# Kernel tuning notes

Hardware: AMD Instinct MI355X
Metric: run time of the kernel (lower is better)

The kernel has to match this reference:

```python
import jax, jax.numpy as jnp
import numpy as np

N, E, NF, EF = 2048, 65536, 128, 64
HID, NH, HD, FF, L = 256, 8, 32, 1024, 4
OUT, MAXN = 1280, 4096


def setup_inputs() -> dict:
    key = jax.random.key(0)
    ks = iter(jax.random.split(key, 64))
    def rn(shape, s=0.02):
        return jax.random.normal(next(ks), shape, jnp.float32) * s
    inp = dict(
        node_features=jax.random.normal(next(ks), (N, NF), jnp.float32),
        edge_features=jax.random.normal(next(ks), (E, EF), jnp.float32),
        edge_index=jax.random.randint(next(ks), (2, E), 0, N),
        W_node=rn((NF, HID)), b_node=jnp.zeros((HID,)),
        W_edge=rn((EF, HID)), b_edge=jnp.zeros((HID,)),
        pos_emb=rn((MAXN, HID), 1.0),
        Wq=rn((L, HID, HID)), bq=jnp.zeros((L, HID)),
        Wk=rn((L, HID, HID)), bk=jnp.zeros((L, HID)),
        Wv=rn((L, HID, HID)), bv=jnp.zeros((L, HID)),
        Wo=rn((L, HID, HID)), bo=jnp.zeros((L, HID)),
        Wep=rn((L, HID, NH)), bep=jnp.zeros((L, NH)),
        Wf1=rn((L, HID, FF)), bf1=jnp.zeros((L, FF)),
        Wf2=rn((L, FF, HID)), bf2=jnp.zeros((L, HID)),
        g1=jnp.ones((L, HID)), be1=jnp.zeros((L, HID)),
        g2=jnp.ones((L, HID)), be2=jnp.zeros((L, HID)),
        g_ln=jnp.ones((HID,)), b_ln=jnp.zeros((HID,)),
        Wp1=rn((HID, HID)), bp1=jnp.zeros((HID,)),
        Wp2=rn((HID, 1)), bp2=jnp.zeros((1,)),
        Wo1=rn((3 * HID, 2 * HID)), bo1=jnp.zeros((2 * HID,)),
        Wo2=rn((2 * HID, OUT)), bo2=jnp.zeros((OUT,)),
    )
    return inp


def _ln(x, g, b, eps=1e-5):
    m = x.mean(-1, keepdims=True)
    v = ((x - m) ** 2).mean(-1, keepdims=True)
    return (x - m) * jax.lax.rsqrt(v + eps) * g + b


def reference(node_features, edge_features, edge_index, W_node, b_node, W_edge,
              b_edge, pos_emb, Wq, bq, Wk, bk, Wv, bv, Wo, bo, Wep, bep,
              Wf1, bf1, Wf2, bf2, g1, be1, g2, be2, g_ln, b_ln,
              Wp1, bp1, Wp2, bp2, Wo1, bo1, Wo2, bo2):
    n = node_features.shape[0]
    src, dst = edge_index[0], edge_index[1]
    scale = float(np.sqrt(HD))
    # node encoding + learned positional embedding (n <= max_nodes path)
    x = node_features @ W_node + b_node + pos_emb[:n]
    edge_attr = edge_features @ W_edge + b_edge  # [E, HID]
    # symmetric adjacency mask with self-loops
    adj = jnp.zeros((n, n), bool).at[src, dst].set(True).at[dst, src].set(True)
    adj = adj.at[jnp.arange(n), jnp.arange(n)].set(True)
    for i in range(L):
        Q = (x @ Wq[i] + bq[i]).reshape(n, NH, HD)
        K = (x @ Wk[i] + bk[i]).reshape(n, NH, HD)
        V = (x @ Wv[i] + bv[i]).reshape(n, NH, HD)
        scores = jnp.einsum('nhd,mhd->nmh', Q, K) / scale  # [n, n, NH]
        ebias = edge_attr @ Wep[i] + bep[i]  # [E, NH]
        scores = scores.at[src, dst].add(ebias)  # accumulating scatter, same as per-edge loop
        scores = jnp.where(adj[:, None, :], scores.transpose(0, 2, 1), -jnp.inf)  # [n, NH, n]
        attn = jax.nn.softmax(scores, axis=-1)
        ctx = jnp.einsum('nhm,mhd->nhd', attn, V).reshape(n, HID)
        a = ctx @ Wo[i] + bo[i]
        x = _ln(x + a, g1[i], be1[i])
        f = jax.nn.gelu(x @ Wf1[i] + bf1[i], approximate=False) @ Wf2[i] + bf2[i]
        x = _ln(x + f, g2[i], be2[i])
    x = _ln(x, g_ln, b_ln)
    # global pooling (batch=None path): mean / max / attention
    mean_p = x.mean(0, keepdims=True)
    max_p = x.max(0, keepdims=True)
    aw = jax.nn.softmax(jnp.tanh(x @ Wp1 + bp1) @ Wp2 + bp2, axis=0)  # [n, 1]
    attn_p = (x * aw).sum(0, keepdims=True)
    g = jnp.concatenate([mean_p, max_p, attn_p], axis=1)  # [1, 3*HID]
    out = jax.nn.relu(g @ Wo1 + bo1) @ Wo2 + bo2  # [1, OUT]
    return out
```

## Files before the change

### kernel.cpp

```cpp
#include <hip/hip_runtime.h>
#include <math.h>

#define NNODE 2048
#define NEDGE 65536
#define HIDN  256
#define NHEAD 8
#define HDIM  32
#define FFD   1024
#define NLAYER 4
#define OUTD  1280
#define NNZ_MAX (2*NEDGE + NNODE)

typedef __attribute__((ext_vector_type(8))) short bf16x8;
typedef __attribute__((ext_vector_type(4))) float f32x4;

__device__ __forceinline__ unsigned short f2b(float f) {
    unsigned u = __float_as_uint(f);
    unsigned r = (u + 0x7fffu + ((u >> 16) & 1u)) >> 16;
    return (unsigned short)r;
}
__device__ __forceinline__ float b2f(unsigned short u) {
    return __uint_as_float((unsigned)u << 16);
}

template<int K, int EPI, int OUT>
__global__ __launch_bounds__(256)
void mgemm(const unsigned short* __restrict__ A, const unsigned short* __restrict__ Bt,
           const float* __restrict__ bias, const float* __restrict__ extra,
           float* __restrict__ Cf, unsigned short* __restrict__ Cb,
           int M, int N, const float* __restrict__ Wp2, float* __restrict__ sred)
{
    __shared__ __align__(16) unsigned short As[2][32 * 40];
    __shared__ __align__(16) unsigned short Bs[2][64 * 40];
    int tid = threadIdx.x;
    int bm0 = blockIdx.y * 32, bn0 = blockIdx.x * 64;
    int wave = tid >> 6, lane = tid & 63;
    int wm = (wave >> 1) * 16;
    int wn = (wave & 1) * 32;
    int lrow = lane & 15, quad = lane >> 4;
    int brow = tid >> 2, koff = (tid & 3) * 8;
    int arow = (tid & 127) >> 2;
    bool doA = tid < 128;
    const unsigned short* ap = A  + (size_t)(bm0 + arow) * K + koff;
    const unsigned short* bp = Bt + (size_t)(bn0 + brow) * K + koff;
    uint4 av, bv;
    if (doA) av = *(const uint4*)ap;
    bv = *(const uint4*)bp;
    constexpr int NC = K / 32;
    if (doA) *(uint4*)(&As[0][arow*40 + koff]) = av;
    *(uint4*)(&Bs[0][brow*40 + koff]) = bv;
    __syncthreads();
    f32x4 acc[2] = {};
    #pragma unroll 8
    for (int c = 0; c < NC; ++c) {
        int cur = c & 1;
        if (c + 1 < NC) {
            if (doA) av = *(const uint4*)(ap + (c+1)*32);
            bv = *(const uint4*)(bp + (c+1)*32);
        }
        bf16x8 af = *(const bf16x8*)(&As[cur][(wm + lrow)*40 + quad*8]);
        bf16x8 b0 = *(const bf16x8*)(&Bs[cur][(wn + lrow)*40 + quad*8]);
        bf16x8 b1 = *(const bf16x8*)(&Bs[cur][(wn + 16 + lrow)*40 + quad*8]);
        acc[0] = __builtin_amdgcn_mfma_f32_16x16x32_bf16(af, b0, acc[0], 0, 0, 0);
        acc[1] = __builtin_amdgcn_mfma_f32_16x16x32_bf16(af, b1, acc[1], 0, 0, 0);
        if (c + 1 < NC) {
            if (doA) *(uint4*)(&As[cur^1][arow*40 + koff]) = av;
            *(uint4*)(&Bs[cur^1][brow*40 + koff]) = bv;
        }
        __syncthreads();
    }
    if (EPI == 4) {
        #pragma unroll
        for (int r = 0; r < 4; r++) {
            int row = bm0 + wm + quad*4 + r;
            float ps = 0.f;
            #pragma unroll
            for (int j = 0; j < 2; j++) {
                int col = bn0 + wn + j*16 + lrow;
                float v = tanhf(acc[j][r] + bias[col]);
                ps += v * Wp2[col];
            }
            ps += __shfl_xor(ps, 1);
            ps += __shfl_xor(ps, 2);
            ps += __shfl_xor(ps, 4);
            ps += __shfl_xor(ps, 8);
            if (lrow == 0) atomicAdd(&sred[row], ps);
        }
        return;
    }
    #pragma unroll
    for (int j = 0; j < 2; j++) {
        int col = bn0 + wn + j*16 + lrow;
        float bvv = bias[col];
        #pragma unroll
        for (int r = 0; r < 4; r++) {
            int row = bm0 + wm + quad*4 + r;
            float v = acc[j][r] + bvv;
            if (EPI == 1) v = 0.5f * v * (1.f + erff(v * 0.70710678118654752f));
            else if (EPI == 3) v += extra[(size_t)row*N + col];
            if (OUT == 0 || OUT == 2) Cf[(size_t)row*N + col] = v;
            if (OUT == 1 || OUT == 2) Cb[(size_t)row*N + col] = f2b(v);
        }
    }
}

__global__ __launch_bounds__(256)
void transpose_all(const float* __restrict__ Wq, const float* __restrict__ Wk,
                   const float* __restrict__ Wv, const float* __restrict__ Wo,
                   const float* __restrict__ Wf1, const float* __restrict__ Wf2,
                   const float* __restrict__ W_node, const float* __restrict__ Wp1,
                   unsigned short* __restrict__ WqkvT, unsigned short* __restrict__ WoT,
                   unsigned short* __restrict__ Wf1T, unsigned short* __restrict__ Wf2T,
                   unsigned short* __restrict__ WnT, unsigned short* __restrict__ Wp1T,
                   const float* __restrict__ nf, unsigned short* __restrict__ nf_b,
                   const float* __restrict__ bq, const float* __restrict__ bk,
                   const float* __restrict__ bv, float* __restrict__ bqkv)
{
    __shared__ unsigned short tile[32][33];
    int bid = blockIdx.x;
    if (bid >= 3168) {
        int t = (bid - 3168) * 256 + threadIdx.x;
        if (t < NNODE*128) {
            nf_b[t] = f2b(nf[t]);
        } else {
            int u = t - NNODE*128;
            if (u < NLAYER*768) {
                int l = u / 768, j = u % 768;
                float vv = (j < 256) ? bq[l*256 + j] : (j < 512 ? bk[l*256 + j - 256] : bv[l*256 + j - 512]);
                bqkv[u] = vv;
            }
        }
        return;
    }
    const float* s; unsigned short* d; int K, N, n0, k0;
    if (bid < 1024) {
        int mat = bid >> 6, rem = bid & 63;
        int m4 = mat & 3, l = mat >> 2;
        s = (m4 == 0 ? Wq : m4 == 1 ? Wk : m4 == 2 ? Wv : Wo) + (size_t)l * 65536;
        d = (m4 < 3) ? WqkvT + (size_t)l*196608 + (size_t)m4*65536
                     : WoT + (size_t)l*65536;
        K = 256; N = 256; n0 = (rem & 7) * 32; k0 = (rem >> 3) * 32;
    } else if (bid < 2048) {
        int idx = bid - 1024; int l = idx >> 8, rem = idx & 255;
        s = Wf1 + (size_t)l*262144; d = Wf1T + (size_t)l*262144;
        K = 256; N = 1024; n0 = (rem & 31) * 32; k0 = (rem >> 5) * 32;
    } else if (bid < 3072) {
        int idx = bid - 2048; int l = idx >> 8, rem = idx & 255;
        s = Wf2 + (size_t)l*262144; d = Wf2T + (size_t)l*262144;
        K = 1024; N = 256; n0 = (rem & 7) * 32; k0 = (rem >> 3) * 32;
    } else if (bid < 3104) {
        int rem = bid - 3072;
        s = W_node; d = WnT;
        K = 128; N = 256; n0 = (rem & 7) * 32; k0 = (rem >> 3) * 32;
    } else {
        int rem = bid - 3104;
        s = Wp1; d = Wp1T;
        K = 256; N = 256; n0 = (rem & 7) * 32; k0 = (rem >> 3) * 32;
    }
    int tx = threadIdx.x & 31, ty = threadIdx.x >> 5;
    #pragma unroll
    for (int i = 0; i < 4; i++)
        tile[ty + i*8][tx] = f2b(s[(size_t)(k0 + ty + i*8) * N + n0 + tx]);
    __syncthreads();
    #pragma unroll
    for (int i = 0; i < 4; i++)
        d[(size_t)(n0 + ty + i*8) * K + k0 + tx] = tile[tx][ty + i*8];
}

__global__ void adj_build(const int* __restrict__ src, const int* __restrict__ dst,
                          unsigned* __restrict__ adjbits)
{
    int t = blockIdx.x * blockDim.x + threadIdx.x;
    if (t < NEDGE) {
        int s = src[t], d = dst[t];
        atomicOr(&adjbits[(size_t)s*64 + (d >> 5)], 1u << (d & 31));
        atomicOr(&adjbits[(size_t)d*64 + (s >> 5)], 1u << (s & 31));
    }
    if (t < NNODE)
        atomicOr(&adjbits[(size_t)t*64 + (t >> 5)], 1u << (t & 31));
}

__global__ void row_rank(const unsigned* __restrict__ adjbits,
                         unsigned* __restrict__ rowcum, int* __restrict__ deg)
{
    int i = blockIdx.x * blockDim.x + threadIdx.x;
    if (i >= NNODE) return;
    unsigned c = 0;
    for (int w = 0; w < 64; w++) {
        rowcum[i*64 + w] = c;
        c += __popc(adjbits[i*64 + w]);
    }
    deg[i] = (int)c;
}

__global__ __launch_bounds__(256)
void scan_kernel(const int* __restrict__ deg, int* __restrict__ rowoff)
{
    __shared__ int part[256];
    int tid = threadIdx.x;
    int base = tid * 8;
    int local[8]; int s = 0;
    #pragma unroll
    for (int k = 0; k < 8; k++) { local[k] = s; s += deg[base + k]; }
    part[tid] = s;
    __syncthreads();
    for (int off = 1; off < 256; off <<= 1) {
        int v = (tid >= off) ? part[tid - off] : 0;
        __syncthreads();
        part[tid] += v;
        __syncthreads();
    }
    int pre = (tid == 0) ? 0 : part[tid - 1];
    #pragma unroll
    for (int k = 0; k < 8; k++) rowoff[base + k] = pre + local[k];
    if (tid == 255) rowoff[NNODE] = part[255];
}

__global__ __launch_bounds__(256)
void fill_cols(const unsigned* __restrict__ adjbits, const int* __restrict__ rowoff,
               const unsigned* __restrict__ rowcum, int* __restrict__ cols)
{
    int t = blockIdx.x * 256 + threadIdx.x;
    int i = t >> 6, w = t & 63;
    unsigned bits = adjbits[(size_t)i*64 + w];
    int base = rowoff[i] + (int)rowcum[(size_t)i*64 + w];
    while (bits) {
        int b = __ffs(bits) - 1;
        cols[base++] = w*32 + b;
        bits &= bits - 1;
    }
}

__global__ void wcomb_kernel(const float* __restrict__ W_edge, const float* __restrict__ b_edge,
                             const float* __restrict__ Wep, const float* __restrict__ bep,
                             float* __restrict__ Wcomb, float* __restrict__ bcomb)
{
    int t = blockIdx.x * blockDim.x + threadIdx.x;
    if (t < 64*32) {
        int k = t >> 5, lh = t & 31, l = lh >> 3, h = lh & 7;
        float acc = 0.f;
        for (int c = 0; c < HIDN; c++)
            acc += W_edge[k*HIDN + c] * Wep[l*HIDN*NHEAD + c*NHEAD + h];
        Wcomb[k*32 + lh] = acc;
    } else if (t < 64*32 + 32) {
        int lh = t - 64*32, l = lh >> 3, h = lh & 7;
        float acc = bep[l*NHEAD + h];
        for (int c = 0; c < HIDN; c++)
            acc += b_edge[c] * Wep[l*HIDN*NHEAD + c*NHEAD + h];
        bcomb[lh] = acc;
    }
}

__global__ __launch_bounds__(256)
void edge_bias_scatter(const float* __restrict__ ef, const float* __restrict__ Wcomb,
                       const float* __restrict__ bcomb,
                       const int* __restrict__ src, const int* __restrict__ dst,
                       const unsigned* __restrict__ adjbits,
                       const unsigned* __restrict__ rowcum,
                       const int* __restrict__ rowoff, float* __restrict__ bias_csr)
{
    __shared__ float Wl[64*32];
    __shared__ float bl[32];
    int tid = threadIdx.x;
    for (int k = tid; k < 64*32; k += 256) Wl[k] = Wcomb[k];
    if (tid < 32) bl[tid] = bcomb[tid];
    __syncthreads();
    int t = blockIdx.x * 256 + tid;
    int e = t >> 5, lh = t & 31;
    const float* f = ef + (size_t)e * 64;
    float acc = bl[lh];
    #pragma unroll
    for (int k = 0; k < 64; k++) acc += f[k] * Wl[k*32 + lh];
    int s = src[e], d = dst[e];
    unsigned wbits = adjbits[(size_t)s*64 + (d >> 5)];
    int rank = (int)rowcum[(size_t)s*64 + (d >> 5)] + __popc(wbits & ((1u << (d & 31)) - 1u));
    int slot = rowoff[s] + rank;
    atomicAdd(&bias_csr[(size_t)slot*32 + lh], acc);
}

__global__ __launch_bounds__(256)
void attn_kernel(const unsigned short* __restrict__ QKVb, const int* __restrict__ rowoff,
                 const int* __restrict__ cols, const float* __restrict__ bias_csr,
                 unsigned short* __restrict__ ctxb, int layer)
{
    __shared__ float mS[4][8], lS[4][8];
    __shared__ __align__(16) float accS[4][256];
    int i = blockIdx.x;
    int tid = threadIdx.x;
    int w = tid >> 6, lane = tid & 63;
    int h = lane >> 3;
    int off = lane * 4;
    ushort4 qu = *(const ushort4*)(QKVb + (size_t)i*768 + off);
    float4 qf = { b2f(qu.x), b2f(qu.y), b2f(qu.z), b2f(qu.w) };
    int start = rowoff[i], end = rowoff[i+1];
    int lh0 = layer * 8 + h;
    float m = -INFINITY, l = 0.f;
    float4 acc = {0.f, 0.f, 0.f, 0.f};
    for (int c0 = start + w; c0 < end; c0 += 256) {
        int myslot = c0 + 4*lane;
        int mycol = (myslot < end) ? cols[myslot] : 0;
        int lim = min(end, c0 + 256);
        int it = 0;
        for (int slot = c0; slot < lim; slot += 4, ++it) {
            int j = __shfl(mycol, it);
            ushort4 ku = *(const ushort4*)(QKVb + (size_t)j*768 + 256 + off);
            float s = qf.x*b2f(ku.x) + qf.y*b2f(ku.y) + qf.z*b2f(ku.z) + qf.w*b2f(ku.w);
            s += __shfl_xor(s, 1);
            s += __shfl_xor(s, 2);
            s += __shfl_xor(s, 4);
            s = s * 0.17677669529663687f + bias_csr[(size_t)slot*32 + lh0];
            float mn = fmaxf(m, s);
            float sc = __expf(m - mn);
            float p  = __expf(s - mn);
            ushort4 vu = *(const ushort4*)(QKVb + (size_t)j*768 + 512 + off);
            acc.x = acc.x*sc + p*b2f(vu.x);
            acc.y = acc.y*sc + p*b2f(vu.y);
            acc.z = acc.z*sc + p*b2f(vu.z);
            acc.w = acc.w*sc + p*b2f(vu.w);
            l = l*sc + p;
            m = mn;
        }
    }
    if ((lane & 7) == 0) { mS[w][h] = m; lS[w][h] = l; }
    *(float4*)&accS[w][off] = acc;
    __syncthreads();
    if (w == 0) {
        float m0 = mS[0][h], m1 = mS[1][h], m2 = mS[2][h], m3 = mS[3][h];
        float mx = fmaxf(fmaxf(m0, m1), fmaxf(m2, m3));
        float e0 = (m0 == -INFINITY) ? 0.f : __expf(m0 - mx);
        float e1 = (m1 == -INFINITY) ? 0.f : __expf(m1 - mx);
        float e2 = (m2 == -INFINITY) ? 0.f : __expf(m2 - mx);
        float e3 = (m3 == -INFINITY) ? 0.f : __expf(m3 - mx);
        float ls = lS[0][h]*e0 + lS[1][h]*e1 + lS[2][h]*e2 + lS[3][h]*e3;
        float4 a0 = *(float4*)&accS[0][off];
        float4 a1 = *(float4*)&accS[1][off];
        float4 a2 = *(float4*)&accS[2][off];
        float4 a3 = *(float4*)&accS[3][off];
        float inv = 1.f / ls;
        ushort4 o;
        o.x = f2b((a0.x*e0 + a1.x*e1 + a2.x*e2 + a3.x*e3) * inv);
        o.y = f2b((a0.y*e0 + a1.y*e1 + a2.y*e2 + a3.y*e3) * inv);
        o.z = f2b((a0.z*e0 + a1.z*e1 + a2.z*e2 + a3.z*e3) * inv);
        o.w = f2b((a0.w*e0 + a1.w*e1 + a2.w*e2 + a3.w*e3) * inv);
        *(ushort4*)(ctxb + (size_t)i*HIDN + off) = o;
    }
}

template<bool RES>
__global__ __launch_bounds__(256)
void ln_kernel(float* __restrict__ x, const float* __restrict__ r,
               const float* __restrict__ g, const float* __restrict__ b,
               unsigned short* __restrict__ xb)
{
    __shared__ float lds[4];
    int row = blockIdx.x, c = threadIdx.x;
    float v = x[(size_t)row*HIDN + c];
    if (RES) v += r[(size_t)row*HIDN + c];
    float s = v;
    for (int mm = 1; mm < 64; mm <<= 1) s += __shfl_xor(s, mm);
    if ((c & 63) == 0) lds[c >> 6] = s;
    __syncthreads();
    float mean = (lds[0] + lds[1] + lds[2] + lds[3]) * (1.f / HIDN);
    __syncthreads();
    float dv = v - mean;
    float qq = dv * dv;
    for (int mm = 1; mm < 64; mm <<= 1) qq += __shfl_xor(qq, mm);
    if ((c & 63) == 0) lds[c >> 6] = qq;
    __syncthreads();
    float var = (lds[0] + lds[1] + lds[2] + lds[3]) * (1.f / HIDN);
    float rs = rsqrtf(var + 1e-5f);
    float o = dv * rs * g[c] + b[c];
    x[(size_t)row*HIDN + c] = o;
    xb[(size_t)row*HIDN + c] = f2b(o);
}

__global__ __launch_bounds__(256)
void pool_part(const float* __restrict__ x, const float* __restrict__ sred,
               float* __restrict__ partial)
{
    __shared__ float red[4];
    __shared__ float aw[128];
    int b = blockIdx.x, tid = threadIdx.x;
    float mxs = -INFINITY;
    for (int r = tid; r < NNODE; r += 256) mxs = fmaxf(mxs, sred[r]);
    for (int mm = 1; mm < 64; mm <<= 1) mxs = fmaxf(mxs, __shfl_xor(mxs, mm));
    if ((tid & 63) == 0) red[tid >> 6] = mxs;
    __syncthreads();
    mxs = fmaxf(fmaxf(red[0], red[1]), fmaxf(red[2], red[3]));
    __syncthreads();
    float ss = 0.f;
    for (int r = tid; r < NNODE; r += 256) ss += __expf(sred[r] - mxs);
    for (int mm = 1; mm < 64; mm <<= 1) ss += __shfl_xor(ss, mm);
    if ((tid & 63) == 0) red[tid >> 6] = ss;
    __syncthreads();
    ss = red[0] + red[1] + red[2] + red[3];
    float inv = 1.f / ss;
    int r0 = b * 128;
    if (tid < 128) aw[tid] = __expf(sred[r0 + tid] - mxs) * inv;
    __syncthreads();
    float sm = 0.f, mx = -INFINITY, ap = 0.f;
    for (int r = 0; r < 128; r++) {
        float v = x[(size_t)(r0 + r)*HIDN + tid];
        sm += v;
        mx = fmaxf(mx, v);
        ap += v * aw[r];
    }
    partial[(size_t)b*768 + tid]       = sm;
    partial[(size_t)b*768 + 256 + tid] = mx;
    partial[(size_t)b*768 + 512 + tid] = ap;
}

__global__ __launch_bounds__(256)
void pool_fin(const float* __restrict__ partial, float* __restrict__ g)
{
    int c = threadIdx.x;
    float sm = 0.f, mx = -INFINITY, ap = 0.f;
    for (int b = 0; b < 16; b++) {
        sm += partial[(size_t)b*768 + c];
        mx = fmaxf(mx, partial[(size_t)b*768 + 256 + c]);
        ap += partial[(size_t)b*768 + 512 + c];
    }
    g[c]          = sm * (1.f / NNODE);
    g[HIDN + c]   = mx;
    g[2*HIDN + c] = ap;
}

__global__ __launch_bounds__(256)
void head1(const float* __restrict__ g, const float* __restrict__ Wo1,
           const float* __restrict__ bo1, float* __restrict__ h1)
{
    __shared__ float hp[4][64];
    int tid = threadIdx.x;
    int w = tid >> 6, lane = tid & 63;
    int j = blockIdx.x * 64 + lane;
    float acc = 0.f;
    int k0 = w * 192;
    for (int k = k0; k < k0 + 192; k++)
        acc += g[k] * Wo1[(size_t)k*512 + j];
    hp[w][lane] = acc;
    __syncthreads();
    if (w == 0) {
        float s = hp[0][lane] + hp[1][lane] + hp[2][lane] + hp[3][lane] + bo1[j];
        h1[j] = fmaxf(s, 0.f);
    }
}

__global__ __launch_bounds__(256)
void head2(const float* __restrict__ h1, const float* __restrict__ Wo2,
           const float* __restrict__ bo2, float* __restrict__ out)
{
    __shared__ float hp[4][64];
    int tid = threadIdx.x;
    int w = tid >> 6, lane = tid & 63;
    int j = blockIdx.x * 64 + lane;
    float acc = 0.f;
    int k0 = w * 128;
    for (int k = k0; k < k0 + 128; k++)
        acc += h1[k] * Wo2[(size_t)k*OUTD + j];
    hp[w][lane] = acc;
    __syncthreads();
    if (w == 0)
        out[j] = hp[0][lane] + hp[1][lane] + hp[2][lane] + hp[3][lane] + bo2[j];
}

extern "C" void kernel_launch(void* const* d_in, const int* in_sizes, int n_in,
                              void* d_out, int out_size, void* d_ws, size_t ws_size,
                              hipStream_t stream)
{
    const float* node_features = (const float*)d_in[0];
    const float* edge_features = (const float*)d_in[1];
    const int*   edge_index    = (const int*)d_in[2];
    const float* W_node = (const float*)d_in[3];
    const float* b_node = (const float*)d_in[4];
    const float* W_edge = (const float*)d_in[5];
    const float* b_edge = (const float*)d_in[6];
    const float* pos_emb = (const float*)d_in[7];
    const float* Wq = (const float*)d_in[8];
    const float* bq = (const float*)d_in[9];
    const float* Wk = (const float*)d_in[10];
    const float* bk = (const float*)d_in[11];
    const float* Wv = (const float*)d_in[12];
    const float* bv = (const float*)d_in[13];
    const float* Wo = (const float*)d_in[14];
    const float* bo = (const float*)d_in[15];
    const float* Wep = (const float*)d_in[16];
    const float* bep = (const float*)d_in[17];
    const float* Wf1 = (const float*)d_in[18];
    const float* bf1 = (const float*)d_in[19];
    const float* Wf2 = (const float*)d_in[20];
    const float* bf2 = (const float*)d_in[21];
    const float* g1  = (const float*)d_in[22];
    const float* be1 = (const float*)d_in[23];
    const float* g2  = (const float*)d_in[24];
    const float* be2 = (const float*)d_in[25];
    const float* g_ln = (const float*)d_in[26];
    const float* b_ln = (const float*)d_in[27];
    const float* Wp1 = (const float*)d_in[28];
    const float* bp1 = (const float*)d_in[29];
    const float* Wp2 = (const float*)d_in[30];
    const float* bp2 = (const float*)d_in[31];
    const float* Wo1 = (const float*)d_in[32];
    const float* bo1 = (const float*)d_in[33];
    const float* Wo2 = (const float*)d_in[34];
    const float* bo2 = (const float*)d_in[35];
    (void)bp2;
    const int* src = edge_index;
    const int* dst = edge_index + NEDGE;

    char* w = (char*)d_ws;
    auto carve = [&](size_t nbytes) {
        void* p = (void*)w;
        w += (nbytes + 255) & ~(size_t)255;
        return p;
    };
    float* x        = (float*)carve((size_t)NNODE*HIDN*4);
    unsigned short* xb = (unsigned short*)carve((size_t)NNODE*HIDN*2);
    unsigned short* bufQKVb = (unsigned short*)carve((size_t)NNODE*768*2);
    float* bufO     = (float*)carve((size_t)NNODE*HIDN*4);
    unsigned short* bufAb = (unsigned short*)carve((size_t)NNODE*HIDN*2);
    unsigned short* bufFb = (unsigned short*)carve((size_t)NNODE*FFD*2);
    float* Wcomb    = (float*)carve(64*32*4);
    float* bcomb    = (float*)carve(32*4);
    unsigned* adjbits = (unsigned*)carve((size_t)NNODE*64*4);
    float* bias_csr = (float*)carve((size_t)NNZ_MAX*32*4);
    float* sbuf  = (float*)carve(NNODE*4);
    unsigned* rowcum  = (unsigned*)carve((size_t)NNODE*64*4);
    int* deg    = (int*)carve(NNODE*4);
    int* rowoff = (int*)carve((NNODE+1)*4);
    int* colsb  = (int*)carve((size_t)NNZ_MAX*4);
    float* gbuf  = (float*)carve(3*HIDN*4);
    float* partial = (float*)carve(16*768*4);
    float* h1buf = (float*)carve(512*4);
    unsigned short* nf_b  = (unsigned short*)carve((size_t)NNODE*128*2);
    unsigned short* WnT   = (unsigned short*)carve((size_t)HIDN*128*2);
    unsigned short* WqkvT = (unsigned short*)carve((size_t)NLAYER*768*HIDN*2);
    float*          bqkv  = (float*)carve((size_t)NLAYER*768*4);
    unsigned short* WoT   = (unsigned short*)carve((size_t)NLAYER*HIDN*HIDN*2);
    unsigned short* Wf1T  = (unsigned short*)carve((size_t)NLAYER*FFD*HIDN*2);
    unsigned short* Wf2T  = (unsigned short*)carve((size_t)NLAYER*HIDN*FFD*2);
    unsigned short* Wp1T  = (unsigned short*)carve((size_t)HIDN*HIDN*2);

    hipMemsetAsync(adjbits, 0,
                   (size_t)NNODE*64*4 + (size_t)NNZ_MAX*32*4 + (size_t)NNODE*4, stream);
    adj_build<<<(NEDGE+255)/256, 256, 0, stream>>>(src, dst, adjbits);
    row_rank<<<NNODE/256, 256, 0, stream>>>(adjbits, rowcum, deg);
    scan_kernel<<<1, 256, 0, stream>>>(deg, rowoff);
    fill_cols<<<(NNODE*64)/256, 256, 0, stream>>>(adjbits, rowoff, rowcum, colsb);
    wcomb_kernel<<<(64*32+32+255)/256, 256, 0, stream>>>(W_edge, b_edge, Wep, bep, Wcomb, bcomb);
    edge_bias_scatter<<<(NEDGE*32)/256, 256, 0, stream>>>(
        edge_features, Wcomb, bcomb, src, dst, adjbits, rowcum, rowoff, bias_csr);

    transpose_all<<<3168 + 1024 + 12, 256, 0, stream>>>(
        Wq, Wk, Wv, Wo, Wf1, Wf2, W_node, Wp1,
        WqkvT, WoT, Wf1T, Wf2T, WnT, Wp1T,
        node_features, nf_b, bq, bk, bv, bqkv);

    mgemm<128,3,2><<<dim3(HIDN/64, NNODE/32), 256, 0, stream>>>(
        nf_b, WnT, b_node, pos_emb, x, xb, NNODE, HIDN, nullptr, nullptr);

    for (int l = 0; l < NLAYER; l++) {
        mgemm<256,0,1><<<dim3(768/64, NNODE/32), 256, 0, stream>>>(
            xb, WqkvT + (size_t)l*768*HIDN, bqkv + l*768, nullptr, nullptr, bufQKVb, NNODE, 768, nullptr, nullptr);
        attn_kernel<<<NNODE, 256, 0, stream>>>(bufQKVb, rowoff, colsb, bias_csr, bufAb, l);
        mgemm<256,0,0><<<dim3(HIDN/64, NNODE/32), 256, 0, stream>>>(
            bufAb, WoT + (size_t)l*HIDN*HIDN, bo + l*HIDN, nullptr, bufO, nullptr, NNODE, HIDN, nullptr, nullptr);
        ln_kernel<true><<<NNODE, 256, 0, stream>>>(x, bufO, g1 + l*HIDN, be1 + l*HIDN, xb);
        mgemm<256,1,1><<<dim3(FFD/64, NNODE/32), 256, 0, stream>>>(
            xb, Wf1T + (size_t)l*FFD*HIDN, bf1 + l*FFD, nullptr, nullptr, bufFb, NNODE, FFD, nullptr, nullptr);
        mgemm<1024,0,0><<<dim3(HIDN/64, NNODE/32), 256, 0, stream>>>(
            bufFb, Wf2T + (size_t)l*HIDN*FFD, bf2 + l*HIDN, nullptr, bufO, nullptr, NNODE, HIDN, nullptr, nullptr);
        ln_kernel<true><<<NNODE, 256, 0, stream>>>(x, bufO, g2 + l*HIDN, be2 + l*HIDN, xb);
    }

    ln_kernel<false><<<NNODE, 256, 0, stream>>>(x, nullptr, g_ln, b_ln, xb);
    mgemm<256,4,0><<<dim3(HIDN/64, NNODE/32), 256, 0, stream>>>(
        xb, Wp1T, bp1, nullptr, nullptr, nullptr, NNODE, HIDN, Wp2, sbuf);
    pool_part<<<16, 256, 0, stream>>>(x, sbuf, partial);
    pool_fin<<<1, 256, 0, stream>>>(partial, gbuf);
    head1<<<8, 256, 0, stream>>>(gbuf, Wo1, bo1, h1buf);
    head2<<<OUTD/64, 256, 0, stream>>>(h1buf, Wo2, bo2, (float*)d_out);
}
```

Before: 453.3 us.

## Fuse residual+LayerNorm into full-row GEMMs and prefetch K/V in attention

Adds a full-row-width (256-column) GEMM kernel that applies bias, the residual add and LayerNorm in its epilogue, including a double-LN variant for the final layer. This replaces the Wo and Wf2 GEMMs together with their separate LN kernels and the final LN launch, removing a round trip of the fp32 intermediate through memory and several launches. The attention loop is also software-pipelined so the next K/V rows and edge bias load while the current one is computed. The trade-off is fewer blocks (64 per GEMM) with lower parallelism and more register pressure.

Measured after the change: 496.7 us. 9.6% more time.

```diff
diff --git a/kernel.cpp b/kernel.cpp
--- a/kernel.cpp
+++ b/kernel.cpp
@@ -102,6 +102,187 @@
             if (OUT == 1 || OUT == 2) Cb[(size_t)row*N + col] = f2b(v);
         }
     }
+}
+
+template<int K, bool DBL>
+__global__ __launch_bounds__(256)
+void mgemm_wide(const unsigned short* __restrict__ A, const unsigned short* __restrict__ Bt,
+                const float* __restrict__ bias, const float* __restrict__ res,
+                const float* __restrict__ ga, const float* __restrict__ ba,
+                const float* __restrict__ gb, const float* __restrict__ bb,
+                float* __restrict__ X, unsigned short* __restrict__ Xb)
+{
+    __shared__ __align__(16) unsigned short As[2][32 * 40];
+    __shared__ __align__(16) unsigned short Bs[2][256 * 40];
+    __shared__ float rsum[4][32], rsq[4][32], rsum2[4][32], rsq2[4][32];
+    int tid = threadIdx.x;
+    int bm0 = blockIdx.x * 32;
+    int w = tid >> 6, lane = tid & 63;
+    int lrow = lane & 15, quad = lane >> 4;
+    int wn = w * 64;
+    int brow = tid >> 2, koff = (tid & 3) * 8;
+    int arow = (tid & 127) >> 2;
+    bool doA = tid < 128;
+    const unsigned short* ap = A + (size_t)(bm0 + arow) * K + koff;
+    const unsigned short* bp0 = Bt + (size_t)brow * K + koff;
+    const unsigned short* bp1 = Bt + (size_t)(brow + 64) * K + koff;
+    const unsigned short* bp2 = Bt + (size_t)(brow + 128) * K + koff;
+    const unsigned short* bp3 = Bt + (size_t)(brow + 192) * K + koff;
+    uint4 av, bv0, bv1, bv2, bv3;
+    if (doA) av = *(const uint4*)ap;
+    bv0 = *(const uint4*)bp0;
+    bv1 = *(const uint4*)bp1;
+    bv2 = *(const uint4*)bp2;
+    bv3 = *(const uint4*)bp3;
+    constexpr int NC = K / 32;
+    if (doA) *(uint4*)(&As[0][arow*40 + koff]) = av;
+    *(uint4*)(&Bs[0][brow*40 + koff])        = bv0;
+    *(uint4*)(&Bs[0][(brow+64)*40 + koff])   = bv1;
+    *(uint4*)(&Bs[0][(brow+128)*40 + koff])  = bv2;
+    *(uint4*)(&Bs[0][(brow+192)*40 + koff])  = bv3;
+    __syncthreads();
+    f32x4 acc[2][4] = {};
+    #pragma unroll 8
+    for (int c = 0; c < NC; ++c) {
+        int cur = c & 1;
+        if (c + 1 < NC) {
+            if (doA) av = *(const uint4*)(ap + (c+1)*32);
+            bv0 = *(const uint4*)(bp0 + (c+1)*32);
+            bv1 = *(const uint4*)(bp1 + (c+1)*32);
+            bv2 = *(const uint4*)(bp2 + (c+1)*32);
+            bv3 = *(const uint4*)(bp3 + (c+1)*32);
+        }
+        bf16x8 af[2], bf[4];
+        #pragma unroll
+        for (int i = 0; i < 2; i++) af[i] = *(const bf16x8*)(&As[cur][(i*16 + lrow)*40 + quad*8]);
+        #pragma unroll
+        for (int j = 0; j < 4; j++) bf[j] = *(const bf16x8*)(&Bs[cur][(wn + j*16 + lrow)*40 + quad*8]);
+        #pragma unroll
+        for (int i = 0; i < 2; i++)
+            #pragma unroll
+            for (int j = 0; j < 4; j++)
+                acc[i][j] = __builtin_amdgcn_mfma_f32_16x16x32_bf16(af[i], bf[j], acc[i][j], 0, 0, 0);
+        if (c + 1 < NC) {
+            if (doA) *(uint4*)(&As[cur^1][arow*40 + koff]) = av;
+            *(uint4*)(&Bs[cur^1][brow*40 + koff])        = bv0;
+            *(uint4*)(&Bs[cur^1][(brow+64)*40 + koff])   = bv1;
+            *(uint4*)(&Bs[cur^1][(brow+128)*40 + koff])  = bv2;
+            *(uint4*)(&Bs[cur^1][(brow+192)*40 + koff])  = bv3;
+        }
+        __syncthreads();
+    }
+    float v[2][4][4];
+    #pragma unroll
+    for (int i = 0; i < 2; i++)
+        #pragma unroll
+        for (int j = 0; j < 4; j++) {
+            int col = wn + j*16 + lrow;
+            float bvv = bias[col];
+            #pragma unroll
+            for (int r = 0; r < 4; r++) {
+                int row_l = i*16 + quad*4 + r;
+                v[i][j][r] = acc[i][j][r] + bvv + res[(size_t)(bm0 + row_l)*HIDN + col];
+            }
+        }
+    float mean[2][4], rsv[2][4];
+    #pragma unroll
+    for (int i = 0; i < 2; i++)
+        #pragma unroll
+        for (int r = 0; r < 4; r++) {
+            float s = v[i][0][r] + v[i][1][r] + v[i][2][r] + v[i][3][r];
+            s += __shfl_xor(s, 1); s += __shfl_xor(s, 2);
+            s += __shfl_xor(s, 4); s += __shfl_xor(s, 8);
+            if (lrow == 0) rsum[w][i*16 + quad*4 + r] = s;
+        }
+    __syncthreads();
+    #pragma unroll
+    for (int i = 0; i < 2; i++)
+        #pragma unroll
+        for (int r = 0; r < 4; r++) {
+            int rl = i*16 + quad*4 + r;
+            mean[i][r] = (rsum[0][rl] + rsum[1][rl] + rsum[2][rl] + rsum[3][rl]) * (1.f/HIDN);
+            float q = 0.f;
+            #pragma unroll
+            for (int j = 0; j < 4; j++) { float d = v[i][j][r] - mean[i][r]; q += d*d; }
+            q += __shfl_xor(q, 1); q += __shfl_xor(q, 2);
+            q += __shfl_xor(q, 4); q += __shfl_xor(q, 8);
+            if (lrow == 0) rsq[w][rl] = q;
+        }
+    __syncthreads();
+    #pragma unroll
+    for (int i = 0; i < 2; i++)
+        #pragma unroll
+        for (int r = 0; r < 4; r++) {
+            int rl = i*16 + quad*4 + r;
+            float var = (rsq[0][rl] + rsq[1][rl] + rsq[2][rl] + rsq[3][rl]) * (1.f/HIDN);
+            rsv[i][r] = rsqrtf(var + 1e-5f);
+        }
+    #pragma unroll
+    for (int i = 0; i < 2; i++)
+        #pragma unroll
+        for (int j = 0; j < 4; j++) {
+            int col = wn + j*16 + lrow;
+            float gv = ga[col], bvv = ba[col];
+            #pragma unroll
+            for (int r = 0; r < 4; r++)
+                v[i][j][r] = (v[i][j][r] - mean[i][r]) * rsv[i][r] * gv + bvv;
+        }
+    if (DBL) {
+        #pragma unroll
+        for (int i = 0; i < 2; i++)
+            #pragma unroll
+            for (int r = 0; r < 4; r++) {
+                float s = v[i][0][r] + v[i][1][r] + v[i][2][r] + v[i][3][r];
+                s += __shfl_xor(s, 1); s += __shfl_xor(s, 2);
+                s += __shfl_xor(s, 4); s += __shfl_xor(s, 8);
+                if (lrow == 0) rsum2[w][i*16 + quad*4 + r] = s;
+            }
+        __syncthreads();
+        #pragma unroll
+        for (int i = 0; i < 2; i++)
+            #pragma unroll
+            for (int r = 0; r < 4; r++) {
+                int rl = i*16 + quad*4 + r;
+                mean[i][r] = (rsum2[0][rl] + rsum2[1][rl] + rsum2[2][rl] + rsum2[3][rl]) * (1.f/HIDN);
+                float q = 0.f;
+                #pragma unroll
+                for (int j = 0; j < 4; j++) { float d = v[i][j][r] - mean[i][r]; q += d*d; }
+                q += __shfl_xor(q, 1); q += __shfl_xor(q, 2);
+                q += __shfl_xor(q, 4); q += __shfl_xor(q, 8);
+                if (lrow == 0) rsq2[w][rl] = q;
+            }
+        __syncthreads();
+        #pragma unroll
+        for (int i = 0; i < 2; i++)
+            #pragma unroll
+            for (int r = 0; r < 4; r++) {
+                int rl = i*16 + quad*4 + r;
+                float var = (rsq2[0][rl] + rsq2[1][rl] + rsq2[2][rl] + rsq2[3][rl]) * (1.f/HIDN);
+                rsv[i][r] = rsqrtf(var + 1e-5f);
+            }
+        #pragma unroll
+        for (int i = 0; i < 2; i++)
+            #pragma unroll
+            for (int j = 0; j < 4; j++) {
+                int col = wn + j*16 + lrow;
+                float gv = gb[col], bvv = bb[col];
+                #pragma unroll
+                for (int r = 0; r < 4; r++)
+                    v[i][j][r] = (v[i][j][r] - mean[i][r]) * rsv[i][r] * gv + bvv;
+            }
+    }
+    #pragma unroll
+    for (int i = 0; i < 2; i++)
+        #pragma unroll
+        for (int j = 0; j < 4; j++) {
+            int col = wn + j*16 + lrow;
+            #pragma unroll
+            for (int r = 0; r < 4; r++) {
+                int row = bm0 + i*16 + quad*4 + r;
+                X[(size_t)row*HIDN + col] = v[i][j][r];
+                Xb[(size_t)row*HIDN + col] = f2b(v[i][j][r]);
+            }
+        }
 }
 
 __global__ __launch_bounds__(256)
@@ -290,6 +471,8 @@
     int w = tid >> 6, lane = tid & 63;
     int h = lane >> 3;
     int off = lane * 4;
+    const unsigned short* Kbase = QKVb + 256 + off;
+    const unsigned short* Vbase = QKVb + 512 + off;
     ushort4 qu = *(const ushort4*)(QKVb + (size_t)i*768 + off);
     float4 qf = { b2f(qu.x), b2f(qu.y), b2f(qu.z), b2f(qu.w) };
     int start = rowoff[i], end = rowoff[i+1];
@@ -300,25 +483,32 @@
         int myslot = c0 + 4*lane;
         int mycol = (myslot < end) ? cols[myslot] : 0;
         int lim = min(end, c0 + 256);
-        int it = 0;
-        for (int slot = c0; slot < lim; slot += 4, ++it) {
-            int j = __shfl(mycol, it);
-            ushort4 ku = *(const ushort4*)(QKVb + (size_t)j*768 + 256 + off);
+        int nit = (lim - c0 + 3) >> 2;
+        int j0 = __shfl(mycol, 0);
+        ushort4 ku = *(const ushort4*)(Kbase + (size_t)j0*768);
+        ushort4 vu = *(const ushort4*)(Vbase + (size_t)j0*768);
+        float bcur = bias_csr[(size_t)c0*32 + lh0];
+        for (int it = 0; it < nit; ++it) {
+            int itn = (it + 1 < nit) ? it + 1 : it;
+            int jn = __shfl(mycol, itn);
+            ushort4 kun = *(const ushort4*)(Kbase + (size_t)jn*768);
+            ushort4 vun = *(const ushort4*)(Vbase + (size_t)jn*768);
+            float bnxt = bias_csr[(size_t)(c0 + 4*itn)*32 + lh0];
             float s = qf.x*b2f(ku.x) + qf.y*b2f(ku.y) + qf.z*b2f(ku.z) + qf.w*b2f(ku.w);
             s += __shfl_xor(s, 1);
             s += __shfl_xor(s, 2);
             s += __shfl_xor(s, 4);
-            s = s * 0.17677669529663687f + bias_csr[(size_t)slot*32 + lh0];
+            s = s * 0.17677669529663687f + bcur;
             float mn = fmaxf(m, s);
             float sc = __expf(m - mn);
             float p  = __expf(s - mn);
-            ushort4 vu = *(const ushort4*)(QKVb + (size_t)j*768 + 512 + off);
             acc.x = acc.x*sc + p*b2f(vu.x);
             acc.y = acc.y*sc + p*b2f(vu.y);
             acc.z = acc.z*sc + p*b2f(vu.z);
             acc.w = acc.w*sc + p*b2f(vu.w);
             l = l*sc + p;
             m = mn;
+            ku = kun; vu = vun; bcur = bnxt;
         }
     }
     if ((lane & 7) == 0) { mS[w][h] = m; lS[w][h] = l; }
@@ -344,34 +534,6 @@
         o.w = f2b((a0.w*e0 + a1.w*e1 + a2.w*e2 + a3.w*e3) * inv);
         *(ushort4*)(ctxb + (size_t)i*HIDN + off) = o;
     }
-}
-
-template<bool RES>
-__global__ __launch_bounds__(256)
-void ln_kernel(float* __restrict__ x, const float* __restrict__ r,
-               const float* __restrict__ g, const float* __restrict__ b,
-               unsigned short* __restrict__ xb)
-{
-    __shared__ float lds[4];
-    int row = blockIdx.x, c = threadIdx.x;
-    float v = x[(size_t)row*HIDN + c];
-    if (RES) v += r[(size_t)row*HIDN + c];
-    float s = v;
-    for (int mm = 1; mm < 64; mm <<= 1) s += __shfl_xor(s, mm);
-    if ((c & 63) == 0) lds[c >> 6] = s;
-    __syncthreads();
-    float mean = (lds[0] + lds[1] + lds[2] + lds[3]) * (1.f / HIDN);
-    __syncthreads();
-    float dv = v - mean;
-    float qq = dv * dv;
-    for (int mm = 1; mm < 64; mm <<= 1) qq += __shfl_xor(qq, mm);
-    if ((c & 63) == 0) lds[c >> 6] = qq;
-    __syncthreads();
-    float var = (lds[0] + lds[1] + lds[2] + lds[3]) * (1.f / HIDN);
-    float rs = rsqrtf(var + 1e-5f);
-    float o = dv * rs * g[c] + b[c];
-    x[(size_t)row*HIDN + c] = o;
-    xb[(size_t)row*HIDN + c] = f2b(o);
 }
 
 __global__ __launch_bounds__(256)
@@ -562,17 +724,21 @@
         mgemm<256,0,1><<<dim3(768/64, NNODE/32), 256, 0, stream>>>(
             xb, WqkvT + (size_t)l*768*HIDN, bqkv + l*768, nullptr, nullptr, bufQKVb, NNODE, 768, nullptr, nullptr);
         attn_kernel<<<NNODE, 256, 0, stream>>>(bufQKVb, rowoff, colsb, bias_csr, bufAb, l);
-        mgemm<256,0,0><<<dim3(HIDN/64, NNODE/32), 256, 0, stream>>>(
-            bufAb, WoT + (size_t)l*HIDN*HIDN, bo + l*HIDN, nullptr, bufO, nullptr, NNODE, HIDN, nullptr, nullptr);
-        ln_kernel<true><<<NNODE, 256, 0, stream>>>(x, bufO, g1 + l*HIDN, be1 + l*HIDN, xb);
+        mgemm_wide<256,false><<<NNODE/32, 256, 0, stream>>>(
+            bufAb, WoT + (size_t)l*HIDN*HIDN, bo + l*HIDN, x,
+            g1 + l*HIDN, be1 + l*HIDN, nullptr, nullptr, x, xb);
         mgemm<256,1,1><<<dim3(FFD/64, NNODE/32), 256, 0, stream>>>(
             xb, Wf1T + (size_t)l*FFD*HIDN, bf1 + l*FFD, nullptr, nullptr, bufFb, NNODE, FFD, nullptr, nullptr);
-        mgemm<1024,0,0><<<dim3(HIDN/64, NNODE/32), 256, 0, stream>>>(
-            bufFb, Wf2T + (size_t)l*HIDN*FFD, bf2 + l*HIDN, nullptr, bufO, nullptr, NNODE, HIDN, nullptr, nullptr);
-        ln_kernel<true><<<NNODE, 256, 0, stream>>>(x, bufO, g2 + l*HIDN, be2 + l*HIDN, xb);
-    }
-
-    ln_kernel<false><<<NNODE, 256, 0, stream>>>(x, nullptr, g_ln, b_ln, xb);
+        if (l < NLAYER - 1)
+            mgemm_wide<1024,false><<<NNODE/32, 256, 0, stream>>>(
+                bufFb, Wf2T + (size_t)l*HIDN*FFD, bf2 + l*HIDN, x,
+                g2 + l*HIDN, be2 + l*HIDN, nullptr, nullptr, x, xb);
+        else
+            mgemm_wide<1024,true><<<NNODE/32, 256, 0, stream>>>(
+                bufFb, Wf2T + (size_t)l*HIDN*FFD, bf2 + l*HIDN, x,
+                g2 + l*HIDN, be2 + l*HIDN, g_ln, b_ln, x, xb);
+    }
+
     mgemm<256,4,0><<<dim3(HIDN/64, NNODE/32), 256, 0, stream>>>(
         xb, Wp1T, bp1, nullptr, nullptr, nullptr, NNODE, HIDN, Wp2, sbuf);
     pool_part<<<16, 256, 0, stream>>>(x, sbuf, partial);
```
